# Optimization experiments

Measured on AMD Instinct MI355X. Metric: run time of the kernel, lower is better.

## Reference

```python
import jax, jax.numpy as jnp
import numpy as np

B, Q, L = 64, 64, 8192
KC = 51            # NarrowConv1D kernel size
HC = KC // 2 + 1   # 26 raw symmetric-half params
N = 500
KT = N + 1         # 501 transpose-conv kernel size
HT = KT // 2 + 1   # 251 raw half params

@jax.custom_vjp
def sigmoid_st(u):
    # Sigmoid forward, straight-through (identity) backward
    return jax.nn.sigmoid(u)

def _sst_fwd(u):
    return jax.nn.sigmoid(u), None

def _sst_bwd(res, g):
    return (g,)

sigmoid_st.defvjp(_sst_fwd, _sst_bwd)

def symmetric(w):
    # cat(X, X[..., :-1].flip(-1)) -> symmetric kernel of odd length
    return jnp.concatenate([w, w[..., :-1][..., ::-1]], axis=-1)

def depthwise_conv(x, k, pad):
    # x: [B, Q, L]; k: [Q, K] one kernel per channel (groups == channels)
    return jax.lax.conv_general_dilated(
        x, k[:, None, :], window_strides=(1,), padding=[(pad, pad)],
        dimension_numbers=("NCH", "OIH", "NCH"), feature_group_count=x.shape[1])

def setup_inputs() -> dict:
    key = jax.random.key(0)
    k1, k2, k3, k4 = jax.random.split(key, 4)
    return {
        "x": jax.random.normal(k1, (B, Q, L), dtype=jnp.float32),
        "conv_w_half": jax.random.normal(k2, (HC,), dtype=jnp.float32) * 0.1,
        "tc_w_half": jax.random.normal(k3, (Q, HT), dtype=jnp.float32),
        "A_raw": jax.random.normal(k4, (Q,), dtype=jnp.float32),
    }

def reference(x, conv_w_half, tc_w_half, A_raw):
    # 1) NarrowConv1D: one symmetric kernel shared across all Q channels
    kc = symmetric(conv_w_half)                       # [51]
    kc_full = jnp.broadcast_to(kc, (Q, KC))           # ChannelSame expand
    x = depthwise_conv(x, kc_full, KC // 2)           # [B,Q,L], 'same'

    # 2) softmax over spectral axis
    x = jax.nn.softmax(x, axis=-1)

    # 3) SymmetricNormConvTranspose1d: sigmoid(straight-through) + symmetric;
    #    stride-1 transpose conv with symmetric kernel == depthwise conv with
    #    padding K-1-p = N//2
    wt = sigmoid_st(tc_w_half)                        # [Q, 251] in (0,1)
    kt = symmetric(wt)                                # [Q, 501]
    x = depthwise_conv(x, kt, N // 2)                 # [B,Q,L]

    # 4) serial lattice (reflection/transmission) recursion over Q channels
    a = sigmoid_st(A_raw)                             # [Q]
    xs = jnp.transpose(x, (1, 0, 2))                  # [Q,B,L]

    def step(carry, inp):
        r, t2 = carry
        rn, aq = inp
        tn = 1.0 - rn
        s = 1.0 / (1.0 - aq * r * rn)
        r_new = r + aq * rn * t2 * s
        t2_new = aq * t2 * tn * tn * s * s
        return (r_new, t2_new), None

    init = (jnp.zeros_like(xs[0]), jnp.ones_like(xs[0]))
    (r, _), _ = jax.lax.scan(step, init, (xs, a))

    peak = wt[-1, -1]                                 # weight[-1,0,N//2] (kernel center)
    r = r / (peak * jnp.prod(a))
    return r                                          # [B, L]
```

## Files before the change

### kernel.cpp

```cpp
#include <hip/hip_runtime.h>

#define B_ 64
#define Q_ 64
#define L_ 8192
#define KCONV 51
#define HC 26
#define HT 251
#define NCH2 34
#define NCH1 6

#define A51_OFF 512
#define TA_OFF  8192
#define RN_OFF  2236416

#define MAPB(s) ((((s) & ~7) | ((((s) & 7) + ((s) >> 3)) & 7)) << 4)

typedef _Float16 f16x8 __attribute__((ext_vector_type(8)));
typedef float f32x16 __attribute__((ext_vector_type(16)));

__device__ __forceinline__ float sigm(float v) {
    return 1.0f / (1.0f + __expf(-v));
}

__global__ __launch_bounds__(256) void k_params(const float* __restrict__ cwh,
                                                const float* __restrict__ tcw,
                                                const float* __restrict__ araw,
                                                float* __restrict__ ws) {
    const int tid = threadIdx.x;
    const int q = blockIdx.x;
    char* wsb = (char*)ws;
    if (q < Q_) {
        for (int idx = tid; idx < NCH2 * 64; idx += 256) {
            int c = idx >> 6, lane = idx & 63;
            int hi = lane >> 5, i = lane & 31;
            int mbase = 16 * c + 8 * hi - i - 6;
            f16x8 hv;
            #pragma unroll
            for (int jj = 0; jj < 8; jj++) {
                int m = mbase + jj;
                float v = 0.0f;
                if (m >= 0 && m <= 500) {
                    int hh = (m <= 250) ? m : (500 - m);
                    v = sigm(tcw[q * HT + hh]);
                }
                hv[jj] = (_Float16)v;
            }
            *(f16x8*)(wsb + TA_OFF + ((size_t)q * (NCH2 * 64) + idx) * 16) = hv;
        }
    } else {
        if (tid < Q_) ws[tid] = sigm(araw[tid]);
        for (int idx = tid; idx < NCH1 * 64; idx += 256) {
            int c = idx >> 6, lane = idx & 63;
            int hi = lane >> 5, i = lane & 31;
            int mbase = 16 * c + 8 * hi - i - 7;
            f16x8 hv;
            #pragma unroll
            for (int jj = 0; jj < 8; jj++) {
                int m = mbase + jj;
                float v = 0.0f;
                if (m >= 0 && m < KCONV) v = cwh[m < HC ? m : (KCONV - 1 - m)];
                hv[jj] = (_Float16)v;
            }
            *(f16x8*)(wsb + A51_OFF + idx * 16) = hv;
        }
        __syncthreads();
        if (tid == 0) {
            float p = 1.0f;
            for (int j = 0; j < Q_; j++) p *= ws[j];
            float peak = sigm(tcw[(Q_ - 1) * HT + 250]);
            ws[64] = 1.0f / (peak * p);
        }
    }
}

__global__ __launch_bounds__(512, 2) void k_fused(const float* __restrict__ x,
                                                  float* __restrict__ ws) {
    const int tid = threadIdx.x;
    const int bid = blockIdx.x;
    const int q = bid >> 6, b = bid & 63;
    const int row = b * Q_ + q;
    char* wsb = (char*)ws;
    __shared__ __attribute__((aligned(128))) char xb[16512];
    __shared__ __attribute__((aligned(128))) char sb[17408];
    __shared__ float red[16];

    const int w = tid >> 6, lane = tid & 63, j = lane & 31, hi = lane >> 5;

    f16x8 a51[NCH1];
    #pragma unroll
    for (int c = 0; c < NCH1; c++)
        a51[c] = *(const f16x8*)(wsb + A51_OFF + (c * 64 + lane) * 16);

    int bofs[NCH2];
    #pragma unroll
    for (int c = 0; c < NCH2; c++) bofs[c] = MAPB(128 * w + 4 * j + 2 * c + hi);

    const uint4 z4 = {0u, 0u, 0u, 0u};
    if (tid < 8) { int s = (tid < 4) ? tid : 1024 + tid; *(uint4*)(xb + MAPB(s)) = z4; }
    if (tid >= 32 && tid < 96) {
        int s = (tid < 64) ? (tid - 32) : (1056 + tid - 64);
        *(uint4*)(sb + MAPB(s)) = z4;
    }

    {
        const float* xrow = x + (size_t)row * L_;
        float4 f0 = *(const float4*)(xrow + 16 * tid);
        float4 f1 = *(const float4*)(xrow + 16 * tid + 4);
        float4 f2 = *(const float4*)(xrow + 16 * tid + 8);
        float4 f3 = *(const float4*)(xrow + 16 * tid + 12);
        union H8 { _Float16 h[8]; uint4 u; } h0, h1;
        h0.h[0] = (_Float16)f0.x; h0.h[1] = (_Float16)f0.y;
        h0.h[2] = (_Float16)f0.z; h0.h[3] = (_Float16)f0.w;
        h0.h[4] = (_Float16)f1.x; h0.h[5] = (_Float16)f1.y;
        h0.h[6] = (_Float16)f1.z; h0.h[7] = (_Float16)f1.w;
        h1.h[0] = (_Float16)f2.x; h1.h[1] = (_Float16)f2.y;
        h1.h[2] = (_Float16)f2.z; h1.h[3] = (_Float16)f2.w;
        h1.h[4] = (_Float16)f3.x; h1.h[5] = (_Float16)f3.y;
        h1.h[6] = (_Float16)f3.z; h1.h[7] = (_Float16)f3.w;
        *(uint4*)(xb + MAPB(2 * tid + 4)) = h0.u;
        *(uint4*)(xb + MAPB(2 * tid + 5)) = h1.u;
    }
    __syncthreads();

    f32x16 acc = {};
    #pragma unroll
    for (int c = 0; c < NCH1; c++) {
        f16x8 bf = *(const f16x8*)(xb + bofs[c]);
        acc = __builtin_amdgcn_mfma_f32_32x32x16_f16(a51[c], bf, acc, 0, 0, 0);
    }

    float mx = -3.402823466e+38f;
    #pragma unroll
    for (int e = 0; e < 16; e++) mx = fmaxf(mx, acc[e]);
    #pragma unroll
    for (int o = 32; o > 0; o >>= 1) mx = fmaxf(mx, __shfl_xor(mx, o));
    if (lane == 0) red[w] = mx;
    __syncthreads();
    mx = red[0];
    #pragma unroll
    for (int i = 1; i < 8; i++) mx = fmaxf(mx, red[i]);
    float sm = 0.0f;
    #pragma unroll
    for (int e = 0; e < 16; e++) { acc[e] = __expf(acc[e] - mx); sm += acc[e]; }
    #pragma unroll
    for (int o = 32; o > 0; o >>= 1) sm += __shfl_xor(sm, o);
    if (lane == 0) red[8 + w] = sm;
    __syncthreads();
    float ssum = red[8];
    #pragma unroll
    for (int i = 1; i < 8; i++) ssum += red[8 + i];
    const float isum = 1.0f / ssum;

    union P4 { _Float16 h[4]; uint2 u; };
    #pragma unroll
    for (int k = 0; k < 4; k++) {
        P4 p;
        #pragma unroll
        for (int d = 0; d < 4; d++) p.h[d] = (_Float16)(acc[4 * k + d] * isum);
        *(uint2*)(sb + MAPB(128 * w + 4 * j + k + 32) + 8 * hi) = p.u;
    }
    __syncthreads();

    const char* tab = wsb + TA_OFF + ((size_t)q * (NCH2 * 64) + lane) * 16;
    f32x16 acc2 = {};
    #pragma unroll
    for (int c = 0; c < NCH2; c++) {
        f16x8 af = *(const f16x8*)(tab + c * 1024);
        f16x8 bf = *(const f16x8*)(sb + bofs[c]);
        acc2 = __builtin_amdgcn_mfma_f32_32x32x16_f16(af, bf, acc2, 0, 0, 0);
    }

    #pragma unroll
    for (int k = 0; k < 4; k++) {
        P4 p;
        #pragma unroll
        for (int d = 0; d < 4; d++) p.h[d] = (_Float16)acc2[4 * k + d];
        *(uint2*)(xb + MAPB(128 * w + 4 * j + k) + 8 * hi) = p.u;
    }
    __syncthreads();
    uint4 r0 = *(uint4*)(xb + MAPB(2 * tid));
    uint4 r1 = *(uint4*)(xb + MAPB(2 * tid + 1));
    char* dst = wsb + RN_OFF + ((size_t)row * L_ + 16 * tid) * 2;
    *(uint4*)dst = r0;
    *(uint4*)(dst + 16) = r1;
}

__global__ __launch_bounds__(256) void k_lat(const float* __restrict__ ws,
                                             float* __restrict__ out) {
    const int tid = threadIdx.x;
    const int T = blockIdx.x & 7, b = blockIdx.x >> 3;
    const char* wsb = (const char*)ws;
    const int l = 1024 * T + 4 * tid;
    const char* src = wsb + RN_OFF + ((size_t)(b * Q_) * L_ + l) * 2;
    float r[4] = {0.0f, 0.0f, 0.0f, 0.0f};
    float t2[4] = {1.0f, 1.0f, 1.0f, 1.0f};
    union P4 { _Float16 h[4]; uint2 u; };
    P4 cur;
    cur.u = *(const uint2*)src;
    for (int q = 0; q < Q_; q++) {
        P4 nxt = cur;
        if (q < Q_ - 1) nxt.u = *(const uint2*)(src + (size_t)(q + 1) * L_ * 2);
        const float aq = ws[q];
        #pragma unroll
        for (int e = 0; e < 4; e++) {
            float rn = (float)cur.h[e], tn = 1.0f - rn;
            float si = 1.0f / (1.0f - aq * r[e] * rn);
            float rnew = r[e] + aq * rn * t2[e] * si;
            t2[e] = aq * t2[e] * tn * tn * si * si;
            r[e] = rnew;
        }
        cur = nxt;
    }
    const float inv_scale = ws[64];
    float4 o;
    o.x = r[0] * inv_scale; o.y = r[1] * inv_scale;
    o.z = r[2] * inv_scale; o.w = r[3] * inv_scale;
    *(float4*)&out[(size_t)b * L_ + l] = o;
}

extern "C" void kernel_launch(void* const* d_in, const int* in_sizes, int n_in,
                              void* d_out, int out_size, void* d_ws, size_t ws_size,
                              hipStream_t stream) {
    (void)in_sizes; (void)n_in; (void)out_size; (void)ws_size;
    const float* x    = (const float*)d_in[0];
    const float* cwh  = (const float*)d_in[1];
    const float* tcw  = (const float*)d_in[2];
    const float* araw = (const float*)d_in[3];
    float* out = (float*)d_out;
    float* ws  = (float*)d_ws;

    hipLaunchKernelGGL(k_params, dim3(Q_ + 1), dim3(256), 0, stream, cwh, tcw, araw, ws);
    hipLaunchKernelGGL(k_fused, dim3(B_ * Q_), dim3(512), 0, stream, x, ws);
    hipLaunchKernelGGL(k_lat, dim3(B_ * 8), dim3(256), 0, stream, ws, out);
}
```

Baseline: 102.6 us.

## Process two batch rows per block and stage transpose-conv weights in LDS

Each block now handles two batch rows for the same channel, so the per-channel 501-tap weight fragments are loaded once and reused across two MFMA accumulator chains. Most weight chunks are copied into LDS with global_load_lds direct loads. The remaining chunks and the 51-tap weights still come from global memory. Launch bounds are raised to 4 blocks per CU and the grid is halved. The cost is roughly 63 KB of LDS per block and extra register pressure from the doubled accumulators, which may make the 4-block occupancy target unreachable.

```diff
diff --git a/kernel.cpp b/kernel.cpp
--- a/kernel.cpp
+++ b/kernel.cpp
@@ -8,6 +8,7 @@
 #define HT 251
 #define NCH2 34
 #define NCH1 6
+#define TAL_CH 28
 
 #define A51_OFF 512
 #define TA_OFF  8192
@@ -17,6 +18,8 @@
 
 typedef _Float16 f16x8 __attribute__((ext_vector_type(8)));
 typedef float f32x16 __attribute__((ext_vector_type(16)));
+typedef const __attribute__((address_space(1))) void cg_void;
+typedef __attribute__((address_space(3))) void lds_void3;
 
 __device__ __forceinline__ float sigm(float v) {
     return 1.0f / (1.0f + __expf(-v));
@@ -73,116 +76,162 @@
     }
 }
 
-__global__ __launch_bounds__(512, 2) void k_fused(const float* __restrict__ x,
+__global__ __launch_bounds__(512, 4) void k_fused(const float* __restrict__ x,
                                                   float* __restrict__ ws) {
     const int tid = threadIdx.x;
     const int bid = blockIdx.x;
-    const int q = bid >> 6, b = bid & 63;
-    const int row = b * Q_ + q;
+    const int q = bid >> 5, pr = bid & 31;
+    const int row0 = (2 * pr) * Q_ + q, row1 = (2 * pr + 1) * Q_ + q;
     char* wsb = (char*)ws;
-    __shared__ __attribute__((aligned(128))) char xb[16512];
-    __shared__ __attribute__((aligned(128))) char sb[17408];
-    __shared__ float red[16];
+    __shared__ __attribute__((aligned(128))) char bufA[17408];
+    __shared__ __attribute__((aligned(128))) char bufB[17408];
+    __shared__ __attribute__((aligned(128))) char TAL[TAL_CH * 1024];
+    __shared__ float red[32];
 
     const int w = tid >> 6, lane = tid & 63, j = lane & 31, hi = lane >> 5;
 
-    f16x8 a51[NCH1];
-    #pragma unroll
-    for (int c = 0; c < NCH1; c++)
-        a51[c] = *(const f16x8*)(wsb + A51_OFF + (c * 64 + lane) * 16);
-
-    int bofs[NCH2];
-    #pragma unroll
-    for (int c = 0; c < NCH2; c++) bofs[c] = MAPB(128 * w + 4 * j + 2 * c + hi);
+    {
+        const char* tabg = wsb + TA_OFF + (size_t)q * (NCH2 * 64) * 16;
+        for (int c = w; c < TAL_CH; c += 8) {
+            const void* gp = tabg + (c * 64 + lane) * 16;
+            __builtin_amdgcn_global_load_lds((cg_void*)gp,
+                                             (lds_void3*)(TAL + c * 1024), 16, 0, 0);
+        }
+    }
 
     const uint4 z4 = {0u, 0u, 0u, 0u};
-    if (tid < 8) { int s = (tid < 4) ? tid : 1024 + tid; *(uint4*)(xb + MAPB(s)) = z4; }
-    if (tid >= 32 && tid < 96) {
-        int s = (tid < 64) ? (tid - 32) : (1056 + tid - 64);
-        *(uint4*)(sb + MAPB(s)) = z4;
-    }
-
-    {
-        const float* xrow = x + (size_t)row * L_;
-        float4 f0 = *(const float4*)(xrow + 16 * tid);
-        float4 f1 = *(const float4*)(xrow + 16 * tid + 4);
-        float4 f2 = *(const float4*)(xrow + 16 * tid + 8);
-        float4 f3 = *(const float4*)(xrow + 16 * tid + 12);
-        union H8 { _Float16 h[8]; uint4 u; } h0, h1;
-        h0.h[0] = (_Float16)f0.x; h0.h[1] = (_Float16)f0.y;
-        h0.h[2] = (_Float16)f0.z; h0.h[3] = (_Float16)f0.w;
-        h0.h[4] = (_Float16)f1.x; h0.h[5] = (_Float16)f1.y;
-        h0.h[6] = (_Float16)f1.z; h0.h[7] = (_Float16)f1.w;
-        h1.h[0] = (_Float16)f2.x; h1.h[1] = (_Float16)f2.y;
-        h1.h[2] = (_Float16)f2.z; h1.h[3] = (_Float16)f2.w;
-        h1.h[4] = (_Float16)f3.x; h1.h[5] = (_Float16)f3.y;
-        h1.h[6] = (_Float16)f3.z; h1.h[7] = (_Float16)f3.w;
-        *(uint4*)(xb + MAPB(2 * tid + 4)) = h0.u;
-        *(uint4*)(xb + MAPB(2 * tid + 5)) = h1.u;
-    }
-    __syncthreads();
-
-    f32x16 acc = {};
-    #pragma unroll
-    for (int c = 0; c < NCH1; c++) {
-        f16x8 bf = *(const f16x8*)(xb + bofs[c]);
-        acc = __builtin_amdgcn_mfma_f32_32x32x16_f16(a51[c], bf, acc, 0, 0, 0);
-    }
-
-    float mx = -3.402823466e+38f;
-    #pragma unroll
-    for (int e = 0; e < 16; e++) mx = fmaxf(mx, acc[e]);
-    #pragma unroll
-    for (int o = 32; o > 0; o >>= 1) mx = fmaxf(mx, __shfl_xor(mx, o));
-    if (lane == 0) red[w] = mx;
-    __syncthreads();
-    mx = red[0];
-    #pragma unroll
-    for (int i = 1; i < 8; i++) mx = fmaxf(mx, red[i]);
-    float sm = 0.0f;
-    #pragma unroll
-    for (int e = 0; e < 16; e++) { acc[e] = __expf(acc[e] - mx); sm += acc[e]; }
-    #pragma unroll
-    for (int o = 32; o > 0; o >>= 1) sm += __shfl_xor(sm, o);
-    if (lane == 0) red[8 + w] = sm;
-    __syncthreads();
-    float ssum = red[8];
-    #pragma unroll
-    for (int i = 1; i < 8; i++) ssum += red[8 + i];
-    const float isum = 1.0f / ssum;
+    if (tid < 32) {
+        *(uint4*)(bufA + MAPB(tid)) = z4;
+        *(uint4*)(bufB + MAPB(tid)) = z4;
+    } else if (tid >= 64 && tid < 96) {
+        int s = 1056 + (tid - 64);
+        *(uint4*)(bufA + MAPB(s)) = z4;
+        *(uint4*)(bufB + MAPB(s)) = z4;
+    }
+
+    union H8 { _Float16 h[8]; uint4 u; };
+    {
+        const float* xr0 = x + (size_t)row0 * L_ + 16 * tid;
+        const float* xr1 = x + (size_t)row1 * L_ + 16 * tid;
+        #pragma unroll
+        for (int r = 0; r < 2; r++) {
+            const float* xr = r ? xr1 : xr0;
+            char* buf = r ? bufB : bufA;
+            float4 f0 = *(const float4*)(xr + 0);
+            float4 f1 = *(const float4*)(xr + 4);
+            float4 f2 = *(const float4*)(xr + 8);
+            float4 f3 = *(const float4*)(xr + 12);
+            H8 h0, h1;
+            h0.h[0] = (_Float16)f0.x; h0.h[1] = (_Float16)f0.y;
+            h0.h[2] = (_Float16)f0.z; h0.h[3] = (_Float16)f0.w;
+            h0.h[4] = (_Float16)f1.x; h0.h[5] = (_Float16)f1.y;
+            h0.h[6] = (_Float16)f1.z; h0.h[7] = (_Float16)f1.w;
+            h1.h[0] = (_Float16)f2.x; h1.h[1] = (_Float16)f2.y;
+            h1.h[2] = (_Float16)f2.z; h1.h[3] = (_Float16)f2.w;
+            h1.h[4] = (_Float16)f3.x; h1.h[5] = (_Float16)f3.y;
+            h1.h[6] = (_Float16)f3.z; h1.h[7] = (_Float16)f3.w;
+            *(uint4*)(buf + MAPB(2 * tid + 32)) = h0.u;
+            *(uint4*)(buf + MAPB(2 * tid + 33)) = h1.u;
+        }
+    }
+    __syncthreads();
+
+    f32x16 acc0 = {}, acc1 = {};
+    {
+        #pragma unroll
+        for (int c = 0; c < NCH1; c++) {
+            f16x8 a51 = *(const f16x8*)(wsb + A51_OFF + (c * 64 + lane) * 16);
+            const int bo = MAPB(128 * w + 4 * j + 2 * c + 28 + hi);
+            f16x8 bf0 = *(const f16x8*)(bufA + bo);
+            f16x8 bf1 = *(const f16x8*)(bufB + bo);
+            acc0 = __builtin_amdgcn_mfma_f32_32x32x16_f16(a51, bf0, acc0, 0, 0, 0);
+            acc1 = __builtin_amdgcn_mfma_f32_32x32x16_f16(a51, bf1, acc1, 0, 0, 0);
+        }
+    }
+
+    float mx0 = -3.402823466e+38f, mx1 = -3.402823466e+38f;
+    #pragma unroll
+    for (int e = 0; e < 16; e++) { mx0 = fmaxf(mx0, acc0[e]); mx1 = fmaxf(mx1, acc1[e]); }
+    #pragma unroll
+    for (int o = 32; o > 0; o >>= 1) {
+        mx0 = fmaxf(mx0, __shfl_xor(mx0, o));
+        mx1 = fmaxf(mx1, __shfl_xor(mx1, o));
+    }
+    if (lane == 0) { red[w] = mx0; red[8 + w] = mx1; }
+    __syncthreads();
+    mx0 = red[0]; mx1 = red[8];
+    #pragma unroll
+    for (int i = 1; i < 8; i++) { mx0 = fmaxf(mx0, red[i]); mx1 = fmaxf(mx1, red[8 + i]); }
+    float sm0 = 0.0f, sm1 = 0.0f;
+    #pragma unroll
+    for (int e = 0; e < 16; e++) {
+        acc0[e] = __expf(acc0[e] - mx0); sm0 += acc0[e];
+        acc1[e] = __expf(acc1[e] - mx1); sm1 += acc1[e];
+    }
+    #pragma unroll
+    for (int o = 32; o > 0; o >>= 1) { sm0 += __shfl_xor(sm0, o); sm1 += __shfl_xor(sm1, o); }
+    if (lane == 0) { red[16 + w] = sm0; red[24 + w] = sm1; }
+    __syncthreads();
+    float s0 = red[16], s1 = red[24];
+    #pragma unroll
+    for (int i = 1; i < 8; i++) { s0 += red[16 + i]; s1 += red[24 + i]; }
+    const float isum0 = 1.0f / s0, isum1 = 1.0f / s1;
 
     union P4 { _Float16 h[4]; uint2 u; };
     #pragma unroll
     for (int k = 0; k < 4; k++) {
-        P4 p;
-        #pragma unroll
-        for (int d = 0; d < 4; d++) p.h[d] = (_Float16)(acc[4 * k + d] * isum);
-        *(uint2*)(sb + MAPB(128 * w + 4 * j + k + 32) + 8 * hi) = p.u;
-    }
-    __syncthreads();
-
-    const char* tab = wsb + TA_OFF + ((size_t)q * (NCH2 * 64) + lane) * 16;
-    f32x16 acc2 = {};
+        P4 p0, p1;
+        #pragma unroll
+        for (int d = 0; d < 4; d++) {
+            p0.h[d] = (_Float16)(acc0[4 * k + d] * isum0);
+            p1.h[d] = (_Float16)(acc1[4 * k + d] * isum1);
+        }
+        const int bo = MAPB(128 * w + 4 * j + k + 32) + 8 * hi;
+        *(uint2*)(bufA + bo) = p0.u;
+        *(uint2*)(bufB + bo) = p1.u;
+    }
+    __syncthreads();
+
+    const char* tab6 = wsb + TA_OFF + ((size_t)q * (NCH2 * 64) + lane) * 16;
+    f32x16 o0 = {}, o1 = {};
     #pragma unroll
     for (int c = 0; c < NCH2; c++) {
-        f16x8 af = *(const f16x8*)(tab + c * 1024);
-        f16x8 bf = *(const f16x8*)(sb + bofs[c]);
-        acc2 = __builtin_amdgcn_mfma_f32_32x32x16_f16(af, bf, acc2, 0, 0, 0);
-    }
+        f16x8 af = (c < TAL_CH)
+            ? *(const f16x8*)(TAL + c * 1024 + lane * 16)
+            : *(const f16x8*)(tab6 + c * 1024);
+        const int bo = MAPB(128 * w + 4 * j + 2 * c + hi);
+        f16x8 bf0 = *(const f16x8*)(bufA + bo);
+        f16x8 bf1 = *(const f16x8*)(bufB + bo);
+        o0 = __builtin_amdgcn_mfma_f32_32x32x16_f16(af, bf0, o0, 0, 0, 0);
+        o1 = __builtin_amdgcn_mfma_f32_32x32x16_f16(af, bf1, o1, 0, 0, 0);
+    }
+    __syncthreads();
 
     #pragma unroll
     for (int k = 0; k < 4; k++) {
-        P4 p;
-        #pragma unroll
-        for (int d = 0; d < 4; d++) p.h[d] = (_Float16)acc2[4 * k + d];
-        *(uint2*)(xb + MAPB(128 * w + 4 * j + k) + 8 * hi) = p.u;
-    }
-    __syncthreads();
-    uint4 r0 = *(uint4*)(xb + MAPB(2 * tid));
-    uint4 r1 = *(uint4*)(xb + MAPB(2 * tid + 1));
-    char* dst = wsb + RN_OFF + ((size_t)row * L_ + 16 * tid) * 2;
-    *(uint4*)dst = r0;
-    *(uint4*)(dst + 16) = r1;
+        P4 p0, p1;
+        #pragma unroll
+        for (int d = 0; d < 4; d++) {
+            p0.h[d] = (_Float16)o0[4 * k + d];
+            p1.h[d] = (_Float16)o1[4 * k + d];
+        }
+        const int bo = MAPB(128 * w + 4 * j + k) + 8 * hi;
+        *(uint2*)(bufA + bo) = p0.u;
+        *(uint2*)(bufB + bo) = p1.u;
+    }
+    __syncthreads();
+    {
+        uint4 r0 = *(uint4*)(bufA + MAPB(2 * tid));
+        uint4 r1 = *(uint4*)(bufA + MAPB(2 * tid + 1));
+        char* dst = wsb + RN_OFF + ((size_t)row0 * L_ + 16 * tid) * 2;
+        *(uint4*)dst = r0;
+        *(uint4*)(dst + 16) = r1;
+        uint4 r2 = *(uint4*)(bufB + MAPB(2 * tid));
+        uint4 r3 = *(uint4*)(bufB + MAPB(2 * tid + 1));
+        char* dst1 = wsb + RN_OFF + ((size_t)row1 * L_ + 16 * tid) * 2;
+        *(uint4*)dst1 = r2;
+        *(uint4*)(dst1 + 16) = r3;
+    }
 }
 
 __global__ __launch_bounds__(256) void k_lat(const float* __restrict__ ws,
@@ -230,6 +279,6 @@
     float* ws  = (float*)d_ws;
 
     hipLaunchKernelGGL(k_params, dim3(Q_ + 1), dim3(256), 0, stream, cwh, tcw, araw, ws);
-    hipLaunchKernelGGL(k_fused, dim3(B_ * Q_), dim3(512), 0, stream, x, ws);
+    hipLaunchKernelGGL(k_fused, dim3((B_ / 2) * Q_), dim3(512), 0, stream, x, ws);
     hipLaunchKernelGGL(k_lat, dim3(B_ * 8), dim3(256), 0, stream, ws, out);
 }
```

After: 97.85 us. 1.05x faster.
